# Optimization experiments

Hardware: AMD Instinct MI355X
Metric: run time of the kernel (lower is better)

## Reference

```python
import jax, jax.numpy as jnp
import numpy as np

N_ADAPTERS = 16
RANK = 16
ALPHA = 16.0
SCALING = ALPHA / RANK
B, S, IN, OUT = 32, 512, 1024, 4096


def setup_inputs() -> dict:
    key = jax.random.key(0)
    k1, k2, k3, k4, k5, k6 = jax.random.split(key, 6)
    hidden_states = jax.random.normal(k1, (B, S, IN), dtype=jnp.float32)
    adapter_ids = jax.random.randint(k2, (B,), 0, N_ADAPTERS, dtype=jnp.int64)
    W = jax.random.normal(k3, (IN, OUT), dtype=jnp.float32) * 0.02
    b = jax.random.normal(k4, (OUT,), dtype=jnp.float32) * 0.02
    lora_a = jax.random.normal(k5, (N_ADAPTERS, IN, RANK), dtype=jnp.float32) * (1.0 / np.sqrt(IN))
    lora_b = jax.random.normal(k6, (N_ADAPTERS, RANK, OUT), dtype=jnp.float32) * 0.02
    return {"hidden_states": hidden_states, "adapter_ids": adapter_ids,
            "W": W, "b": b, "lora_a": lora_a, "lora_b": lora_b}


def reference(hidden_states, adapter_ids, W, b, lora_a, lora_b):
    # Base Conv1D (GPT-2 style): x @ W + b  -> [B, S, OUT]
    base_output = jnp.einsum('bsi,io->bso', hidden_states, W) + b
    # Per-sample adapter gather (replaces the unique-id loop + boolean masks):
    a_sel = lora_a[adapter_ids]          # [B, IN, R]
    b_sel = lora_b[adapter_ids]          # [B, R, OUT]
    low_rank = jnp.einsum('bsi,bir->bsr', hidden_states, a_sel)   # [B, S, R]
    delta = jnp.einsum('bsr,bro->bso', low_rank, b_sel) * SCALING # [B, S, OUT]
    return base_output + delta
```

## Files before the change

kernel.cpp:

```cpp
#include <hip/hip_runtime.h>

#define M_TOT 16384
#define N_TOT 4096
#define K_TOT 1024
#define R_LORA 16
#define NSTEP 64

typedef __attribute__((ext_vector_type(8))) short bf16x8_t;
typedef __attribute__((ext_vector_type(4))) float f32x4_t;

__device__ __forceinline__ unsigned short f2bf(float f) {
  unsigned u = __builtin_bit_cast(unsigned, f);
  u += 0x7FFFu + ((u >> 16) & 1u);
  return (unsigned short)(u >> 16);
}

__device__ __forceinline__ void gload_lds16(const void* g, void* l) {
  __builtin_amdgcn_global_load_lds(
      (const __attribute__((address_space(1))) unsigned int*)g,
      (__attribute__((address_space(3))) unsigned int*)l, 16, 0, 0);
}

__global__ __launch_bounds__(256) void prep_kernel(const float* __restrict__ x,
                                                   const float* __restrict__ W,
                                                   const float* __restrict__ lora_a,
                                                   const float* __restrict__ lora_b,
                                                   unsigned short* __restrict__ xB,
                                                   unsigned short* __restrict__ WtB,
                                                   unsigned short* __restrict__ AtB,
                                                   unsigned short* __restrict__ lbT) {
  __shared__ float lds[64][65];
  const int bid = blockIdx.x;
  const int t = threadIdx.x;
  if (bid < 1024) {
    size_t i = (size_t)bid * 256 + t;
    const size_t stride = (size_t)1024 * 256;
    const size_t n4 = (size_t)M_TOT * K_TOT / 4;
    for (; i < n4; i += stride) {
      float4 v = ((const float4*)x)[i];
      ushort4 h;
      h.x = f2bf(v.x); h.y = f2bf(v.y); h.z = f2bf(v.z); h.w = f2bf(v.w);
      ((ushort4*)xB)[i] = h;
    }
  } else if (bid < 2048) {
    const int v = bid - 1024;
    const int k0 = (v & 15) * 64;
    const int n0 = (v >> 4) * 64;
    const int rr = t >> 4;
    const int cc = (t & 15) * 4;
#pragma unroll
    for (int i = 0; i < 4; ++i) {
      int row = i * 16 + rr;
      float4 w4 = *(const float4*)(W + (size_t)(k0 + row) * N_TOT + n0 + cc);
      lds[row][cc + 0] = w4.x; lds[row][cc + 1] = w4.y;
      lds[row][cc + 2] = w4.z; lds[row][cc + 3] = w4.w;
    }
    __syncthreads();
#pragma unroll
    for (int i = 0; i < 4; ++i) {
      int nrow = i * 16 + rr;
      ushort4 h;
      h.x = f2bf(lds[cc + 0][nrow]); h.y = f2bf(lds[cc + 1][nrow]);
      h.z = f2bf(lds[cc + 2][nrow]); h.w = f2bf(lds[cc + 3][nrow]);
      *(ushort4*)(WtB + (size_t)(n0 + nrow) * K_TOT + k0 + cc) = h;
    }
  } else {
    const int b2 = bid - 2048;
    if (b2 < 64) {
      int idx = b2 * 256 + t;
      int aid = idx >> 10;
      int k = idx & 1023;
      const float* src = lora_a + (size_t)idx * 16;
#pragma unroll
      for (int q = 0; q < 4; ++q) {
        float4 v4 = ((const float4*)src)[q];
#pragma unroll
        for (int j = 0; j < 4; ++j) {
          int r = q * 4 + j;
          float val = (j == 0) ? v4.x : (j == 1) ? v4.y : (j == 2) ? v4.z : v4.w;
          AtB[(((size_t)aid * 16 + r) << 10) + k] = f2bf(val);
        }
      }
    } else {
      int idx = (b2 - 64) * 256 + t;
      int aid = idx >> 12;
      int n = idx & 4095;
      unsigned short o[16];
#pragma unroll
      for (int r = 0; r < 16; ++r)
        o[r] = f2bf(lora_b[((size_t)aid * 16 + r) * N_TOT + n]);
      ushort4* dst = (ushort4*)(lbT + ((size_t)aid * N_TOT + n) * 16);
#pragma unroll
      for (int q = 0; q < 4; ++q) {
        ushort4 h; h.x = o[q*4+0]; h.y = o[q*4+1]; h.z = o[q*4+2]; h.w = o[q*4+3];
        dst[q] = h;
      }
    }
  }
}

__global__ __launch_bounds__(256) void lowrank_kernel(const unsigned short* __restrict__ xB,
                                                      const unsigned short* __restrict__ AtB,
                                                      const int* __restrict__ aids,
                                                      unsigned short* __restrict__ lrB) {
  __shared__ char As[64 * 128];
  const int blk = blockIdx.x;
  const int t = threadIdx.x;
  const int lane = t & 63;
  const int w = t >> 6;
  const int fr = lane & 15, fq = lane >> 4;
  const int aid = aids[blk >> 3];

  const unsigned short* aSrc[2];
  char* aDst[2];
#pragma unroll
  for (int r = 0; r < 2; ++r) {
    int off = (r * 256 + t) * 16;
    int row = off >> 7, cb = off & 127;
    int sb = cb ^ ((row & 7) << 4);
    aSrc[r] = xB + (size_t)(blk * 64 + row) * K_TOT + (sb >> 1);
    aDst[r] = As + off;
  }
  const unsigned short* bBase = AtB + ((size_t)aid * 16 + fr) * K_TOT + fq * 8;

  f32x4_t acc = (f32x4_t){0.f, 0.f, 0.f, 0.f};

  for (int kt = 0; kt < 16; ++kt) {
#pragma unroll
    for (int r = 0; r < 2; ++r) gload_lds16(aSrc[r] + kt * 64, aDst[r]);
    __syncthreads();
#pragma unroll
    for (int ks = 0; ks < 2; ++ks) {
      bf16x8_t bfr = *(const bf16x8_t*)(bBase + kt * 64 + ks * 32);
      int row = w * 16 + fr;
      int cb = ks * 64 + fq * 16;
      bf16x8_t af = *(const bf16x8_t*)(As + row * 128 + (cb ^ ((row & 7) << 4)));
      acc = __builtin_amdgcn_mfma_f32_16x16x32_bf16(af, bfr, acc, 0, 0, 0);
    }
    __syncthreads();
  }
  {
    int gm0 = blk * 64 + w * 16 + fq * 4;
#pragma unroll
    for (int q = 0; q < 4; ++q)
      lrB[(size_t)(gm0 + q) * R_LORA + fr] = f2bf(acc[q]);
  }
}

#define STAGE_HALF(gbase, koff, ldsbase)                                   \
  do {                                                                     \
    gload_lds16((const char*)(gbase) + (koff), (ldsbase) + t * 16);        \
    gload_lds16((const char*)(gbase) + 64 * 2048 + (koff),                 \
                (ldsbase) + 8192 + t * 16);                                \
  } while (0)

#define MM(AS, BS, MH, NH)                                                 \
  do {                                                                     \
    _Pragma("unroll") for (int ks = 0; ks < 2; ++ks)                       \
      _Pragma("unroll") for (int m = 0; m < 4; ++m)                        \
        _Pragma("unroll") for (int n = 0; n < 2; ++n)                      \
          acc[(MH) * 4 + m][(NH) * 2 + n] =                                \
              __builtin_amdgcn_mfma_f32_16x16x32_bf16(                     \
                  AS[m][ks], BS[n][ks],                                    \
                  acc[(MH) * 4 + m][(NH) * 2 + n], 0, 0, 0);               \
  } while (0)

__global__ __launch_bounds__(512, 2) void gemm_kernel(
    const unsigned short* __restrict__ xB, const unsigned short* __restrict__ WtB,
    const unsigned short* __restrict__ lrB, const unsigned short* __restrict__ lbT,
    const float* __restrict__ bias, const int* __restrict__ aids,
    float* __restrict__ out) {
  __shared__ char smem[131072];

  const int orig = blockIdx.x;
  const int xcd = orig & 7;
  const int j = orig >> 3;
  const int tn = xcd * 2 + (j & 1);
  const int tmg = j >> 1;

  const int t = threadIdx.x;
  const int lane = t & 63;
  const int wid = t >> 6;
  const int wr = wid >> 2;
  const int wc = wid & 3;
  const int fr = lane & 15, fq = lane >> 4;

  const int laneA = fr * 128 + (((fq << 4) ^ ((fr & 7) << 4)));
  const int waveAoff = wr * 16384;
  const int waveBoff = 32768 + (wc >> 1) * 16384 + (wc & 1) * 8192;

  const int srow = t >> 3;
  const int sb = (((t & 7) ^ (srow & 7)) << 4);
  const char* pAbase = (const char*)xB + (size_t)(tmg * 1024 + srow) * 2048 + sb;
  const char* pBpanel = (const char*)WtB + (size_t)(tn * 256 + srow) * 2048 + sb;

  f32x4_t acc[8][4];
#pragma unroll
  for (int m = 0; m < 8; ++m)
#pragma unroll
    for (int n = 0; n < 4; ++n) acc[m][n] = (f32x4_t){0.f, 0.f, 0.f, 0.f};

  STAGE_HALF(pAbase, 0, smem + 0);
  STAGE_HALF(pAbase + (size_t)128 * 2048, 0, smem + 16384);
  STAGE_HALF(pBpanel, 0, smem + 32768);
  STAGE_HALF(pBpanel + (size_t)128 * 2048, 0, smem + 49152);
  __syncthreads();

#pragma unroll 1
  for (int s = 0; s < NSTEP; ++s) {
    char* base = smem + ((s & 1) << 16);
    char* nbase = smem + (((s + 1) & 1) << 16);
    char* bufA = base + waveAoff;
    char* bufB = base + waveBoff;

    const int u1 = s + 1;
    if (u1 < NSTEP) {
      const char* pA1 = pAbase + (size_t)(u1 >> 4) * (256 * 2048);
      const int k1 = (u1 & 15) * 128;
      STAGE_HALF(pA1, k1, nbase + 0);
      STAGE_HALF(pA1 + (size_t)128 * 2048, k1, nbase + 16384);
      STAGE_HALF(pBpanel, k1, nbase + 32768);
      STAGE_HALF(pBpanel + (size_t)128 * 2048, k1, nbase + 49152);
    }

    bf16x8_t a0F[4][2], a1F[4][2], b0F[2][2], b1F[2][2];
#pragma unroll
    for (int n = 0; n < 2; ++n)
#pragma unroll
      for (int ks = 0; ks < 2; ++ks)
        b0F[n][ks] = *(const bf16x8_t*)(bufB + n * 2048 + (laneA ^ (ks << 6)));
#pragma unroll
    for (int m = 0; m < 4; ++m)
#pragma unroll
      for (int ks = 0; ks < 2; ++ks)
        a0F[m][ks] = *(const bf16x8_t*)(bufA + m * 2048 + (laneA ^ (ks << 6)));
#pragma unroll
    for (int n = 0; n < 2; ++n)
#pragma unroll
      for (int ks = 0; ks < 2; ++ks)
        b1F[n][ks] = *(const bf16x8_t*)(bufB + 4096 + n * 2048 + (laneA ^ (ks << 6)));
#pragma unroll
    for (int m = 0; m < 4; ++m)
#pragma unroll
      for (int ks = 0; ks < 2; ++ks)
        a1F[m][ks] = *(const bf16x8_t*)(bufA + 8192 + m * 2048 + (laneA ^ (ks << 6)));

    MM(a0F, b0F, 0, 0);
    MM(a0F, b1F, 0, 1);
    MM(a1F, b1F, 1, 1);
    MM(a1F, b0F, 1, 0);

    if ((s & 15) == 15) {
      const int tm = tmg * 4 + (s >> 4);
      const int aid = aids[tm >> 1];
      bf16x8_t z8 = (bf16x8_t){0, 0, 0, 0, 0, 0, 0, 0};
      bf16x8_t lrf[8], lbf[4];
#pragma unroll
      for (int m = 0; m < 8; ++m) lrf[m] = z8;
#pragma unroll
      for (int n = 0; n < 4; ++n) lbf[n] = z8;
      if (fq < 2) {
#pragma unroll
        for (int m = 0; m < 8; ++m)
          lrf[m] = *(const bf16x8_t*)(lrB + (size_t)(tm * 256 + wr * 128 + m * 16 + fr) * R_LORA + fq * 8);
#pragma unroll
        for (int n = 0; n < 4; ++n)
          lbf[n] = *(const bf16x8_t*)(lbT + ((size_t)aid * N_TOT + tn * 256 + wc * 64 + n * 16 + fr) * R_LORA + fq * 8);
      }
#pragma unroll
      for (int m = 0; m < 8; ++m)
#pragma unroll
        for (int n = 0; n < 4; ++n)
          acc[m][n] = __builtin_amdgcn_mfma_f32_16x16x32_bf16(lrf[m], lbf[n], acc[m][n], 0, 0, 0);

#pragma unroll
      for (int n = 0; n < 4; ++n) {
        int gn = tn * 256 + wc * 64 + n * 16 + fr;
        float bv = bias[gn];
#pragma unroll
        for (int m = 0; m < 8; ++m) {
          int gm0 = tm * 256 + wr * 128 + m * 16 + fq * 4;
          float* op = out + (size_t)gm0 * N_TOT + gn;
#pragma unroll
          for (int q = 0; q < 4; ++q) op[(size_t)q * N_TOT] = acc[m][n][q] + bv;
        }
      }
#pragma unroll
      for (int m = 0; m < 8; ++m)
#pragma unroll
        for (int n = 0; n < 4; ++n) acc[m][n] = (f32x4_t){0.f, 0.f, 0.f, 0.f};
    }

    __syncthreads();
  }
}

extern "C" void kernel_launch(void* const* d_in, const int* in_sizes, int n_in,
                              void* d_out, int out_size, void* d_ws, size_t ws_size,
                              hipStream_t stream) {
  const float* x      = (const float*)d_in[0];
  const int*   aids   = (const int*)d_in[1];
  const float* W      = (const float*)d_in[2];
  const float* bias   = (const float*)d_in[3];
  const float* lora_a = (const float*)d_in[4];
  const float* lora_b = (const float*)d_in[5];
  float* out = (float*)d_out;

  char* ws = (char*)d_ws;
  unsigned short* xB  = (unsigned short*)(ws);
  unsigned short* WtB = (unsigned short*)(ws + (size_t)32 * 1024 * 1024);
  unsigned short* lrB = (unsigned short*)(ws + (size_t)40 * 1024 * 1024);
  unsigned short* AtB = (unsigned short*)(ws + (size_t)40 * 1024 * 1024 + 512 * 1024);
  unsigned short* lbT = (unsigned short*)(ws + (size_t)41 * 1024 * 1024);

  prep_kernel<<<2368, 256, 0, stream>>>(x, W, lora_a, lora_b, xB, WtB, AtB, lbT);
  lowrank_kernel<<<256, 256, 0, stream>>>(xB, AtB, aids, lrB);
  gemm_kernel<<<256, 512, 0, stream>>>(xB, WtB, lrB, lbT, bias, aids, out);
}
```

Measured before the change: 203.3 us.

## Replace persistent 256x256 GEMM tiles with 128x128 tiles over a 4096-block grid

The base GEMM moves from 256 persistent blocks of 512 threads, each walking four 256x256 output tiles along M, to 4096 blocks of 256 threads, each computing one 128x128 tile. LDS use per block halves and each wave's accumulator shrinks from 8x4 to 4x4 MFMA fragments. The aim is more blocks and waves resident per CU, so latency is hidden better and tail imbalance shrinks. In exchange each tile has lower arithmetic intensity, so more global and L2 traffic is needed per FLOP, and the B panel is no longer reused across consecutive M tiles.

```diff
diff --git a/kernel.cpp b/kernel.cpp
--- a/kernel.cpp
+++ b/kernel.cpp
@@ -4,7 +4,7 @@
 #define N_TOT 4096
 #define K_TOT 1024
 #define R_LORA 16
-#define NSTEP 64
+#define NT 16
 
 typedef __attribute__((ext_vector_type(8))) short bf16x8_t;
 typedef __attribute__((ext_vector_type(4))) float f32x4_t;
@@ -147,151 +147,126 @@
   }
 }
 
-#define STAGE_HALF(gbase, koff, ldsbase)                                   \
-  do {                                                                     \
-    gload_lds16((const char*)(gbase) + (koff), (ldsbase) + t * 16);        \
-    gload_lds16((const char*)(gbase) + 64 * 2048 + (koff),                 \
-                (ldsbase) + 8192 + t * 16);                                \
-  } while (0)
-
-#define MM(AS, BS, MH, NH)                                                 \
-  do {                                                                     \
-    _Pragma("unroll") for (int ks = 0; ks < 2; ++ks)                       \
-      _Pragma("unroll") for (int m = 0; m < 4; ++m)                        \
-        _Pragma("unroll") for (int n = 0; n < 2; ++n)                      \
-          acc[(MH) * 4 + m][(NH) * 2 + n] =                                \
-              __builtin_amdgcn_mfma_f32_16x16x32_bf16(                     \
-                  AS[m][ks], BS[n][ks],                                    \
-                  acc[(MH) * 4 + m][(NH) * 2 + n], 0, 0, 0);               \
-  } while (0)
-
-__global__ __launch_bounds__(512, 2) void gemm_kernel(
+__global__ __launch_bounds__(256, 2) void gemm_kernel(
     const unsigned short* __restrict__ xB, const unsigned short* __restrict__ WtB,
     const unsigned short* __restrict__ lrB, const unsigned short* __restrict__ lbT,
     const float* __restrict__ bias, const int* __restrict__ aids,
     float* __restrict__ out) {
-  __shared__ char smem[131072];
+  __shared__ char smem[65536];
 
   const int orig = blockIdx.x;
   const int xcd = orig & 7;
   const int j = orig >> 3;
-  const int tn = xcd * 2 + (j & 1);
-  const int tmg = j >> 1;
+  const int tn = xcd * 4 + (j & 3);
+  const int tm = j >> 2;
 
   const int t = threadIdx.x;
   const int lane = t & 63;
   const int wid = t >> 6;
-  const int wr = wid >> 2;
-  const int wc = wid & 3;
+  const int wr = wid >> 1;
+  const int wc = wid & 1;
   const int fr = lane & 15, fq = lane >> 4;
 
   const int laneA = fr * 128 + (((fq << 4) ^ ((fr & 7) << 4)));
-  const int waveAoff = wr * 16384;
-  const int waveBoff = 32768 + (wc >> 1) * 16384 + (wc & 1) * 8192;
-
-  const int srow = t >> 3;
-  const int sb = (((t & 7) ^ (srow & 7)) << 4);
-  const char* pAbase = (const char*)xB + (size_t)(tmg * 1024 + srow) * 2048 + sb;
-  const char* pBpanel = (const char*)WtB + (size_t)(tn * 256 + srow) * 2048 + sb;
-
-  f32x4_t acc[8][4];
-#pragma unroll
-  for (int m = 0; m < 8; ++m)
+  const int waveAoff = wr * 8192;
+  const int waveBoff = 16384 + wc * 8192;
+
+  const char* aSrc[4];
+  const char* bSrc[4];
+  char* aDst[4];
+  char* bDst[4];
+#pragma unroll
+  for (int r = 0; r < 4; ++r) {
+    int off = (r * 256 + t) * 16;
+    int row = off >> 7, cb = off & 127;
+    int sb = cb ^ ((row & 7) << 4);
+    aSrc[r] = (const char*)xB + (size_t)(tm * 128 + row) * 2048 + sb;
+    bSrc[r] = (const char*)WtB + (size_t)(tn * 128 + row) * 2048 + sb;
+    aDst[r] = smem + off;
+    bDst[r] = smem + 16384 + off;
+  }
+
+  f32x4_t acc[4][4];
+#pragma unroll
+  for (int m = 0; m < 4; ++m)
 #pragma unroll
     for (int n = 0; n < 4; ++n) acc[m][n] = (f32x4_t){0.f, 0.f, 0.f, 0.f};
 
-  STAGE_HALF(pAbase, 0, smem + 0);
-  STAGE_HALF(pAbase + (size_t)128 * 2048, 0, smem + 16384);
-  STAGE_HALF(pBpanel, 0, smem + 32768);
-  STAGE_HALF(pBpanel + (size_t)128 * 2048, 0, smem + 49152);
+#pragma unroll
+  for (int r = 0; r < 4; ++r) gload_lds16(aSrc[r], aDst[r]);
+#pragma unroll
+  for (int r = 0; r < 4; ++r) gload_lds16(bSrc[r], bDst[r]);
   __syncthreads();
 
 #pragma unroll 1
-  for (int s = 0; s < NSTEP; ++s) {
-    char* base = smem + ((s & 1) << 16);
-    char* nbase = smem + (((s + 1) & 1) << 16);
+  for (int s = 0; s < NT; ++s) {
+    char* base = smem + ((s & 1) << 15);
+    const int nb = (((s + 1) & 1) << 15);
     char* bufA = base + waveAoff;
     char* bufB = base + waveBoff;
 
-    const int u1 = s + 1;
-    if (u1 < NSTEP) {
-      const char* pA1 = pAbase + (size_t)(u1 >> 4) * (256 * 2048);
-      const int k1 = (u1 & 15) * 128;
-      STAGE_HALF(pA1, k1, nbase + 0);
-      STAGE_HALF(pA1 + (size_t)128 * 2048, k1, nbase + 16384);
-      STAGE_HALF(pBpanel, k1, nbase + 32768);
-      STAGE_HALF(pBpanel + (size_t)128 * 2048, k1, nbase + 49152);
-    }
-
-    bf16x8_t a0F[4][2], a1F[4][2], b0F[2][2], b1F[2][2];
-#pragma unroll
-    for (int n = 0; n < 2; ++n)
+    if (s + 1 < NT) {
+      const int k1 = (s + 1) * 128;
+#pragma unroll
+      for (int r = 0; r < 4; ++r) gload_lds16(aSrc[r] + k1, aDst[r] + nb);
+#pragma unroll
+      for (int r = 0; r < 4; ++r) gload_lds16(bSrc[r] + k1, bDst[r] + nb);
+    }
+
+    bf16x8_t aF[4][2], bF[4][2];
+#pragma unroll
+    for (int m = 0; m < 4; ++m)
 #pragma unroll
       for (int ks = 0; ks < 2; ++ks)
-        b0F[n][ks] = *(const bf16x8_t*)(bufB + n * 2048 + (laneA ^ (ks << 6)));
+        aF[m][ks] = *(const bf16x8_t*)(bufA + m * 2048 + (laneA ^ (ks << 6)));
+#pragma unroll
+    for (int n = 0; n < 4; ++n)
+#pragma unroll
+      for (int ks = 0; ks < 2; ++ks)
+        bF[n][ks] = *(const bf16x8_t*)(bufB + n * 2048 + (laneA ^ (ks << 6)));
+
+#pragma unroll
+    for (int ks = 0; ks < 2; ++ks)
+#pragma unroll
+      for (int m = 0; m < 4; ++m)
+#pragma unroll
+        for (int n = 0; n < 4; ++n)
+          acc[m][n] = __builtin_amdgcn_mfma_f32_16x16x32_bf16(
+              aF[m][ks], bF[n][ks], acc[m][n], 0, 0, 0);
+
+    __syncthreads();
+  }
+
+  const int aid = aids[tm >> 2];
+  bf16x8_t z8 = (bf16x8_t){0, 0, 0, 0, 0, 0, 0, 0};
+  bf16x8_t lrf[4], lbf[4];
+#pragma unroll
+  for (int m = 0; m < 4; ++m) { lrf[m] = z8; lbf[m] = z8; }
+  if (fq < 2) {
 #pragma unroll
     for (int m = 0; m < 4; ++m)
-#pragma unroll
-      for (int ks = 0; ks < 2; ++ks)
-        a0F[m][ks] = *(const bf16x8_t*)(bufA + m * 2048 + (laneA ^ (ks << 6)));
-#pragma unroll
-    for (int n = 0; n < 2; ++n)
-#pragma unroll
-      for (int ks = 0; ks < 2; ++ks)
-        b1F[n][ks] = *(const bf16x8_t*)(bufB + 4096 + n * 2048 + (laneA ^ (ks << 6)));
-#pragma unroll
-    for (int m = 0; m < 4; ++m)
-#pragma unroll
-      for (int ks = 0; ks < 2; ++ks)
-        a1F[m][ks] = *(const bf16x8_t*)(bufA + 8192 + m * 2048 + (laneA ^ (ks << 6)));
-
-    MM(a0F, b0F, 0, 0);
-    MM(a0F, b1F, 0, 1);
-    MM(a1F, b1F, 1, 1);
-    MM(a1F, b0F, 1, 0);
-
-    if ((s & 15) == 15) {
-      const int tm = tmg * 4 + (s >> 4);
-      const int aid = aids[tm >> 1];
-      bf16x8_t z8 = (bf16x8_t){0, 0, 0, 0, 0, 0, 0, 0};
-      bf16x8_t lrf[8], lbf[4];
-#pragma unroll
-      for (int m = 0; m < 8; ++m) lrf[m] = z8;
-#pragma unroll
-      for (int n = 0; n < 4; ++n) lbf[n] = z8;
-      if (fq < 2) {
-#pragma unroll
-        for (int m = 0; m < 8; ++m)
-          lrf[m] = *(const bf16x8_t*)(lrB + (size_t)(tm * 256 + wr * 128 + m * 16 + fr) * R_LORA + fq * 8);
-#pragma unroll
-        for (int n = 0; n < 4; ++n)
-          lbf[n] = *(const bf16x8_t*)(lbT + ((size_t)aid * N_TOT + tn * 256 + wc * 64 + n * 16 + fr) * R_LORA + fq * 8);
-      }
-#pragma unroll
-      for (int m = 0; m < 8; ++m)
-#pragma unroll
-        for (int n = 0; n < 4; ++n)
-          acc[m][n] = __builtin_amdgcn_mfma_f32_16x16x32_bf16(lrf[m], lbf[n], acc[m][n], 0, 0, 0);
-
-#pragma unroll
-      for (int n = 0; n < 4; ++n) {
-        int gn = tn * 256 + wc * 64 + n * 16 + fr;
-        float bv = bias[gn];
-#pragma unroll
-        for (int m = 0; m < 8; ++m) {
-          int gm0 = tm * 256 + wr * 128 + m * 16 + fq * 4;
-          float* op = out + (size_t)gm0 * N_TOT + gn;
-#pragma unroll
-          for (int q = 0; q < 4; ++q) op[(size_t)q * N_TOT] = acc[m][n][q] + bv;
-        }
-      }
-#pragma unroll
-      for (int m = 0; m < 8; ++m)
-#pragma unroll
-        for (int n = 0; n < 4; ++n) acc[m][n] = (f32x4_t){0.f, 0.f, 0.f, 0.f};
-    }
-
-    __syncthreads();
+      lrf[m] = *(const bf16x8_t*)(lrB + (size_t)(tm * 128 + wr * 64 + m * 16 + fr) * R_LORA + fq * 8);
+#pragma unroll
+    for (int n = 0; n < 4; ++n)
+      lbf[n] = *(const bf16x8_t*)(lbT + ((size_t)aid * N_TOT + tn * 128 + wc * 64 + n * 16 + fr) * R_LORA + fq * 8);
+  }
+#pragma unroll
+  for (int m = 0; m < 4; ++m)
+#pragma unroll
+    for (int n = 0; n < 4; ++n)
+      acc[m][n] = __builtin_amdgcn_mfma_f32_16x16x32_bf16(lrf[m], lbf[n], acc[m][n], 0, 0, 0);
+
+#pragma unroll
+  for (int n = 0; n < 4; ++n) {
+    int gn = tn * 128 + wc * 64 + n * 16 + fr;
+    float bv = bias[gn];
+#pragma unroll
+    for (int m = 0; m < 4; ++m) {
+      int gm0 = tm * 128 + wr * 64 + m * 16 + fq * 4;
+      float* op = out + (size_t)gm0 * N_TOT + gn;
+#pragma unroll
+      for (int q = 0; q < 4; ++q) op[(size_t)q * N_TOT] = acc[m][n][q] + bv;
+    }
   }
 }
 
@@ -315,5 +290,5 @@
 
   prep_kernel<<<2368, 256, 0, stream>>>(x, W, lora_a, lora_b, xB, WtB, AtB, lbT);
   lowrank_kernel<<<256, 256, 0, stream>>>(xB, AtB, aids, lrB);
-  gemm_kernel<<<256, 512, 0, stream>>>(xB, WtB, lrB, lbT, bias, aids, out);
-}
+  gemm_kernel<<<4096, 256, 0, stream>>>(xB, WtB, lrB, lbT, bias, aids, out);
+}
```

New measurement: 205.9 us. About the same (+1.3%).
